# Performance work log

Measured on AMD Instinct MI355X. Metric: run time of the kernel, lower is better.

Reference implementation:

```python
import jax, jax.numpy as jnp
import numpy as np


def setup_inputs() -> dict:
    key = jax.random.key(0)
    ks = jax.random.split(key, 9)
    N, C, SY, SX = 256, 128, 11, 25
    DM, DC, D = 64, 64, 128
    return {
        "f_t_global": jax.random.normal(ks[0], (N, D), dtype=jnp.float32),
        "x_t_local": jax.random.normal(ks[1], (N, C, SY, SX), dtype=jnp.float32),
        "x_t_prev_local": jax.random.normal(ks[2], (N, C, SY, SX), dtype=jnp.float32),
        "m_t": jax.random.normal(ks[3], (N, DM), dtype=jnp.float32),
        "m_t_prev": jax.random.normal(ks[4], (N, DM), dtype=jnp.float32),
        "c_t": jax.random.normal(ks[5], (N, DC), dtype=jnp.float32),
        "c_t_prev": jax.random.normal(ks[6], (N, DC), dtype=jnp.float32),
        "W_join": jax.random.normal(ks[7], (C + DM + DC, D), dtype=jnp.float32) * 0.05,
        "b_join": jax.random.normal(ks[8], (D,), dtype=jnp.float32) * 0.05,
    }


def reference(f_t_global, x_t_local, x_t_prev_local, m_t, m_t_prev, c_t, c_t_prev, W_join, b_join):
    N, C, SY, SX = x_t_local.shape
    P = SY * SX
    DM = m_t.shape[1]
    # join_obs(local, m, c) = concat([local, m, c]) @ W_join + b_join, split for efficiency
    Wl = W_join[:C]                 # [C, D]
    Wm = W_join[C:C + DM]           # [DM, D]
    Wc = W_join[C + DM:]            # [DC, D]
    # [N, C, SY, SX] -> [P, N, C]: all spatial positions batched at once
    loc_t = x_t_local.reshape(N, C, P).transpose(2, 0, 1)
    loc_p = x_t_prev_local.reshape(N, C, P).transpose(2, 0, 1)
    bias_t = m_t @ Wm + c_t @ Wc + b_join             # [N, D], shared across positions
    bias_p = m_t_prev @ Wm + c_t_prev @ Wc + b_join   # [N, D]
    positive = jnp.einsum('pnc,cd->pnd', loc_p, Wl) + bias_p[None]  # [P, N, D]
    pred_loc = jnp.einsum('pnc,cd->pnd', loc_t, Wl) + bias_t[None]  # [P, N, D]

    # loss1: global prediction vs per-position prev-local positives
    logits1 = jnp.einsum('nd,pmd->pnm', f_t_global, positive)   # [P, N, N]
    # loss2: per-position current-local vs per-position prev-local
    logits2 = jnp.einsum('pnd,pmd->pnm', pred_loc, positive)    # [P, N, N]

    def mean_infonce(logits):
        # cross_entropy(logits, arange(N)) averaged over batch, then over positions
        lse = jax.nn.logsumexp(logits, axis=-1)            # [P, N]
        diag = jnp.diagonal(logits, axis1=1, axis2=2)      # [P, N]
        return jnp.mean(lse - diag)

    loss1 = mean_infonce(logits1)
    loss2 = mean_infonce(logits2)
    return loss1 + loss2
```

## Files before the change

kernel.cpp:

```cpp
#include <hip/hip_runtime.h>

#define Nn 256
#define Cc 128
#define Pp 275
#define Dd 128

typedef unsigned int u32;
typedef unsigned short u16;
typedef float f32x4 __attribute__((ext_vector_type(4)));
typedef short bf16x8 __attribute__((ext_vector_type(8)));

__device__ __forceinline__ float bf2f(u16 h) {
    return __uint_as_float(((u32)h) << 16);
}
__device__ __forceinline__ u16 f2bf(float f) {
    u32 u = __float_as_uint(f);
    return (u16)((u + 0x7fffu + ((u >> 16) & 1u)) >> 16);
}

__global__ __launch_bounds__(256) void bias_kernel(
    const float* __restrict__ m_t, const float* __restrict__ m_p,
    const float* __restrict__ c_t, const float* __restrict__ c_p,
    const float* __restrict__ W, const float* __restrict__ b,
    const float* __restrict__ f,
    float* __restrict__ bias_t, float* __restrict__ bias_p,
    u16* __restrict__ f_bf, u16* __restrict__ WlT)
{
    int idx = blockIdx.x * 256 + threadIdx.x;
    int n = idx >> 7, d = idx & 127;
    float at = 0.f, ap = 0.f;
#pragma unroll 8
    for (int k = 0; k < 64; ++k) {
        float wm = W[(128 + k) * 128 + d];
        float wc = W[(192 + k) * 128 + d];
        at = fmaf(m_t[n * 64 + k], wm, at);
        at = fmaf(c_t[n * 64 + k], wc, at);
        ap = fmaf(m_p[n * 64 + k], wm, ap);
        ap = fmaf(c_p[n * 64 + k], wc, ap);
    }
    float bb = b[d];
    bias_t[idx] = at + bb;
    bias_p[idx] = ap + bb;
    f_bf[idx] = f2bf(f[idx]);
    if (idx < 16384) {
        int dd = idx >> 7, cc = idx & 127;
        WlT[idx] = f2bf(W[cc * 128 + dd]);
    }
}

__global__ __launch_bounds__(512) void join_kernel512(
    const float* __restrict__ x_t, const float* __restrict__ x_p,
    const u16* __restrict__ WlT,
    const float* __restrict__ bias_t, const float* __restrict__ bias_p,
    u16* __restrict__ pred, u16* __restrict__ pos)
{
    __shared__ u16 lds[128 * 128];
    const int tid = threadIdx.x;
    const int n = blockIdx.x;
    const int w = tid >> 6;
    const int l = tid & 63;

    {
        const uint4* src = reinterpret_cast<const uint4*>(WlT);
#pragma unroll
        for (int it = 0; it < 4; ++it) {
            int j = tid + 512 * it;
            int row = j >> 4;
            int colb = (j & 15) << 4;
            uint4 v = src[j];
            *reinterpret_cast<uint4*>((char*)lds + row * 256 + (colb ^ ((row & 7) << 4))) = v;
        }
    }

    float bvT[8], bvP[8];
#pragma unroll
    for (int dt = 0; dt < 8; ++dt) {
        int d = dt * 16 + (l & 15);
        bvT[dt] = bias_t[n * 128 + d];
        bvP[dt] = bias_p[n * 128 + d];
    }

    __syncthreads();

    const float* xbase_t = x_t + (size_t)n * (Cc * Pp);
    const float* xbase_p = x_p + (size_t)n * (Cc * Pp);
    const int cg = (l >> 4) << 3;

    for (int t = w; t < 18; t += 8) {
        const int p0 = t * 16;
        int prow = p0 + (l & 15);
        if (prow > Pp - 1) prow = Pp - 1;
        const float* xs_t = xbase_t + prow;
        const float* xs_p = xbase_p + prow;

        bf16x8 At[4], Ap[4];
#pragma unroll
        for (int kk = 0; kk < 4; ++kk) {
            const size_t cb = (size_t)(kk * 32 + cg) * Pp;
            float vt[8], vp[8];
#pragma unroll
            for (int e = 0; e < 8; ++e) vt[e] = xs_t[cb + (size_t)e * Pp];
#pragma unroll
            for (int e = 0; e < 8; ++e) vp[e] = xs_p[cb + (size_t)e * Pp];
            bf16x8 a, c;
#pragma unroll
            for (int e = 0; e < 8; ++e) { a[e] = (short)f2bf(vt[e]); c[e] = (short)f2bf(vp[e]); }
            At[kk] = a;
            Ap[kk] = c;
        }

#pragma unroll
        for (int dt = 0; dt < 8; ++dt) {
            bf16x8 B[4];
            const int row = dt * 16 + (l & 15);
#pragma unroll
            for (int kk = 0; kk < 4; ++kk) {
                int cbyte = kk * 64 + ((l >> 4) << 4);
                B[kk] = *reinterpret_cast<const bf16x8*>(
                    (const char*)lds + row * 256 + (cbyte ^ ((row & 7) << 4)));
            }
            f32x4 aT = {0.f, 0.f, 0.f, 0.f}, aP = {0.f, 0.f, 0.f, 0.f};
#pragma unroll
            for (int kk = 0; kk < 4; ++kk) {
                aT = __builtin_amdgcn_mfma_f32_16x16x32_bf16(At[kk], B[kk], aT, 0, 0, 0);
                aP = __builtin_amdgcn_mfma_f32_16x16x32_bf16(Ap[kk], B[kk], aP, 0, 0, 0);
            }
            const int d = dt * 16 + (l & 15);
#pragma unroll
            for (int r = 0; r < 4; ++r) {
                int p = p0 + ((l >> 4) << 2) + r;
                if (p < Pp) {
                    size_t o = ((size_t)p * Nn + n) * Dd + d;
                    pred[o] = f2bf(aT[r] + bvT[dt]);
                    pos[o]  = f2bf(aP[r] + bvP[dt]);
                }
            }
        }
    }
}

__global__ __launch_bounds__(512) void logits_mfma_kernel(
    const u16* __restrict__ f_bf,
    const u16* __restrict__ pred, const u16* __restrict__ pos,
    float* __restrict__ partial)
{
    __shared__ u16 lds[Nn * Dd];
    const int tid = threadIdx.x;
    const int sel = blockIdx.x;
    const int p = blockIdx.y;
    const int w = tid >> 6;
    const int l = tid & 63;
    const int r0 = w * 32;

    {
        const uint4* src = reinterpret_cast<const uint4*>(pos + (size_t)p * (Nn * Dd));
#pragma unroll
        for (int it = 0; it < 8; ++it) {
            int j = tid + 512 * it;
            int row = j >> 4;
            int colb = (j & 15) << 4;
            uint4 v = src[j];
            *reinterpret_cast<uint4*>((char*)lds + row * 256 + (colb ^ ((row & 7) << 4))) = v;
        }
    }

    const u16* Abase = sel ? (pred + (size_t)p * (Nn * Dd)) : f_bf;
    bf16x8 A[2][4];
    {
        const int arow = l & 15;
        const int acol = (l >> 4) << 4;
#pragma unroll
        for (int rt = 0; rt < 2; ++rt)
#pragma unroll
            for (int kk = 0; kk < 4; ++kk) {
                const char* ap = (const char*)Abase
                               + (size_t)(r0 + rt * 16 + arow) * 256 + kk * 64 + acol;
                A[rt][kk] = *reinterpret_cast<const bf16x8*>(ap);
            }
    }

    __syncthreads();

    const float L2E = 1.4426950408889634f;
    float s_[2][4];
    float dg[2][4];
#pragma unroll
    for (int rt = 0; rt < 2; ++rt)
#pragma unroll
        for (int r = 0; r < 4; ++r) { s_[rt][r] = 0.f; dg[rt][r] = 0.f; }

    const int mcol = l & 15;
    const int bcol = (l >> 4) << 4;

    for (int ct = 0; ct < 16; ++ct) {
        bf16x8 B[4];
        const int mrow = ct * 16 + mcol;
#pragma unroll
        for (int kk = 0; kk < 4; ++kk) {
            int cb = kk * 64 + bcol;
            B[kk] = *reinterpret_cast<const bf16x8*>(
                (const char*)lds + mrow * 256 + (cb ^ ((mrow & 7) << 4)));
        }
#pragma unroll
        for (int rt = 0; rt < 2; ++rt) {
            f32x4 acc = {0.f, 0.f, 0.f, 0.f};
#pragma unroll
            for (int kk = 0; kk < 4; ++kk)
                acc = __builtin_amdgcn_mfma_f32_16x16x32_bf16(A[rt][kk], B[kk], acc, 0, 0, 0);
            const bool isdg_ct = (ct == ((r0 >> 4) + rt));
#pragma unroll
            for (int r = 0; r < 4; ++r) {
                float v = acc[r];
                s_[rt][r] += __builtin_amdgcn_exp2f(fmaf(v, L2E, -64.f));
                if (isdg_ct && ((l & 15) == (((l >> 4) << 2) + r))) dg[rt][r] = v;
            }
        }
    }

    float local = 0.f;
#pragma unroll
    for (int rt = 0; rt < 2; ++rt)
#pragma unroll
        for (int r = 0; r < 4; ++r) {
            float s = s_[rt][r];
            s += __shfl_xor(s, 1);
            s += __shfl_xor(s, 2);
            s += __shfl_xor(s, 4);
            s += __shfl_xor(s, 8);
            if ((l & 15) == (((l >> 4) << 2) + r))
                local += 0.6931471805599453f * (64.f + __log2f(s)) - dg[rt][r];
        }

    __syncthreads();
    float* red = reinterpret_cast<float*>(lds);
    red[tid] = local;
    __syncthreads();
    for (int k = 256; k > 0; k >>= 1) {
        if (tid < k) red[tid] += red[tid + k];
        __syncthreads();
    }
    if (tid == 0) partial[p * 2 + sel] = red[0];
}

__global__ __launch_bounds__(256) void reduce_kernel(
    const float* __restrict__ partial, float* __restrict__ out)
{
    __shared__ float red[256];
    float s = 0.f;
    for (int i = threadIdx.x; i < 2 * Pp; i += 256) s += partial[i];
    red[threadIdx.x] = s;
    __syncthreads();
    for (int k = 128; k > 0; k >>= 1) {
        if (threadIdx.x < k) red[threadIdx.x] += red[threadIdx.x + k];
        __syncthreads();
    }
    if (threadIdx.x == 0) out[0] = red[0] * (1.0f / (Pp * (float)Nn));
}

extern "C" void kernel_launch(void* const* d_in, const int* in_sizes, int n_in,
                              void* d_out, int out_size, void* d_ws, size_t ws_size,
                              hipStream_t stream)
{
    const float* f   = (const float*)d_in[0];
    const float* x_t = (const float*)d_in[1];
    const float* x_p = (const float*)d_in[2];
    const float* m_t = (const float*)d_in[3];
    const float* m_p = (const float*)d_in[4];
    const float* c_t = (const float*)d_in[5];
    const float* c_p = (const float*)d_in[6];
    const float* W   = (const float*)d_in[7];
    const float* b   = (const float*)d_in[8];

    char* ws = (char*)d_ws;
    const size_t SLAB = (size_t)Pp * Nn * Dd;

    float* bias_t = (float*)ws;
    float* bias_p = bias_t + Nn * Dd;
    u16* f_bf = (u16*)(ws + 262144);
    u16* WlT  = f_bf + Nn * Dd;
    u16* pred = (u16*)(ws + 360448);
    u16* pos  = pred + SLAB;
    float* partial = (float*)(pos + SLAB);

    bias_kernel<<<dim3(Nn * Dd / 256), 256, 0, stream>>>(m_t, m_p, c_t, c_p, W, b, f,
                                                         bias_t, bias_p, f_bf, WlT);
    join_kernel512<<<dim3(Nn), 512, 0, stream>>>(x_t, x_p, WlT, bias_t, bias_p,
                                                 pred, pos);
    logits_mfma_kernel<<<dim3(2, Pp), 512, 0, stream>>>(f_bf, pred, pos, partial);
    reduce_kernel<<<1, 256, 0, stream>>>(partial, (float*)d_out);
}
```

Baseline: 68.57 us.

## Software-pipeline join tile loads and merge both losses into one logits block

The join kernel is unrolled into explicit tile stages, so the global fp32 loads for the next spatial tile are issued before the MFMA work of the current tile, hiding load latency. The logits kernel now handles both losses for a position in a single block, with alternating waves taking loss1 and loss2 over 64 rows each. Each positive slab is therefore staged into LDS once instead of twice, and the grid shrinks by half. In exchange, register pressure rises from the prefetch buffers and the doubled A fragments, which may lower occupancy.

```diff
diff --git a/kernel.cpp b/kernel.cpp
--- a/kernel.cpp
+++ b/kernel.cpp
@@ -48,7 +48,70 @@
     }
 }
 
-__global__ __launch_bounds__(512) void join_kernel512(
+#define LOAD_TILE(vt, vp, t)                                          \
+    {                                                                 \
+        int prow_ = (t) * 16 + (l & 15);                              \
+        if (prow_ > Pp - 1) prow_ = Pp - 1;                           \
+        const float* xst_ = xb_t + prow_;                             \
+        const float* xsp_ = xb_p + prow_;                             \
+        _Pragma("unroll")                                             \
+        for (int kk = 0; kk < 4; ++kk) {                              \
+            const size_t cb_ = (size_t)(kk * 32 + cg) * Pp;           \
+            _Pragma("unroll")                                         \
+            for (int e = 0; e < 8; ++e) {                             \
+                vt[kk * 8 + e] = xst_[cb_ + (size_t)e * Pp];          \
+                vp[kk * 8 + e] = xsp_[cb_ + (size_t)e * Pp];          \
+            }                                                         \
+        }                                                             \
+    }
+
+#define CONV_TILE(At, Ap, vt, vp)                                     \
+    _Pragma("unroll")                                                 \
+    for (int kk = 0; kk < 4; ++kk) {                                  \
+        bf16x8 a_, c_;                                                \
+        _Pragma("unroll")                                             \
+        for (int e = 0; e < 8; ++e) {                                 \
+            a_[e] = (short)f2bf(vt[kk * 8 + e]);                      \
+            c_[e] = (short)f2bf(vp[kk * 8 + e]);                      \
+        }                                                             \
+        At[kk] = a_;                                                  \
+        Ap[kk] = c_;                                                  \
+    }
+
+#define COMPUTE_TILE(At, Ap, t)                                       \
+    {                                                                 \
+        const int p0_ = (t) * 16;                                     \
+        _Pragma("unroll")                                             \
+        for (int dt = 0; dt < 8; ++dt) {                              \
+            bf16x8 B_[4];                                             \
+            const int row_ = dt * 16 + (l & 15);                      \
+            _Pragma("unroll")                                         \
+            for (int kk = 0; kk < 4; ++kk) {                          \
+                int cbyte_ = kk * 64 + ((l >> 4) << 4);               \
+                B_[kk] = *reinterpret_cast<const bf16x8*>(            \
+                    (const char*)lds + row_ * 256 +                   \
+                    (cbyte_ ^ ((row_ & 7) << 4)));                    \
+            }                                                         \
+            f32x4 aT_ = {0.f,0.f,0.f,0.f}, aP_ = {0.f,0.f,0.f,0.f};   \
+            _Pragma("unroll")                                         \
+            for (int kk = 0; kk < 4; ++kk) {                          \
+                aT_ = __builtin_amdgcn_mfma_f32_16x16x32_bf16(At[kk], B_[kk], aT_, 0, 0, 0); \
+                aP_ = __builtin_amdgcn_mfma_f32_16x16x32_bf16(Ap[kk], B_[kk], aP_, 0, 0, 0); \
+            }                                                         \
+            const int d_ = dt * 16 + (l & 15);                        \
+            _Pragma("unroll")                                         \
+            for (int r = 0; r < 4; ++r) {                             \
+                int p_ = p0_ + ((l >> 4) << 2) + r;                   \
+                if (p_ < Pp) {                                        \
+                    size_t o_ = ((size_t)p_ * Nn + n) * Dd + d_;      \
+                    pred[o_] = f2bf(aT_[r] + bvT[dt]);                \
+                    pos[o_]  = f2bf(aP_[r] + bvP[dt]);                \
+                }                                                     \
+            }                                                         \
+        }                                                             \
+    }
+
+__global__ __launch_bounds__(512) void join_pipe_kernel(
     const float* __restrict__ x_t, const float* __restrict__ x_p,
     const u16* __restrict__ WlT,
     const float* __restrict__ bias_t, const float* __restrict__ bias_p,
@@ -72,6 +135,15 @@
         }
     }
 
+    const float* xb_t = x_t + (size_t)n * (Cc * Pp);
+    const float* xb_p = x_p + (size_t)n * (Cc * Pp);
+    const int cg = (l >> 4) << 3;
+
+    float vt0[32], vp0[32], vt1[32], vp1[32], vt2[32], vp2[32];
+    bf16x8 At0[4], Ap0[4], At1[4], Ap1[4], At2[4], Ap2[4];
+
+    LOAD_TILE(vt0, vp0, w);
+
     float bvT[8], bvP[8];
 #pragma unroll
     for (int dt = 0; dt < 8; ++dt) {
@@ -82,60 +154,15 @@
 
     __syncthreads();
 
-    const float* xbase_t = x_t + (size_t)n * (Cc * Pp);
-    const float* xbase_p = x_p + (size_t)n * (Cc * Pp);
-    const int cg = (l >> 4) << 3;
-
-    for (int t = w; t < 18; t += 8) {
-        const int p0 = t * 16;
-        int prow = p0 + (l & 15);
-        if (prow > Pp - 1) prow = Pp - 1;
-        const float* xs_t = xbase_t + prow;
-        const float* xs_p = xbase_p + prow;
-
-        bf16x8 At[4], Ap[4];
-#pragma unroll
-        for (int kk = 0; kk < 4; ++kk) {
-            const size_t cb = (size_t)(kk * 32 + cg) * Pp;
-            float vt[8], vp[8];
-#pragma unroll
-            for (int e = 0; e < 8; ++e) vt[e] = xs_t[cb + (size_t)e * Pp];
-#pragma unroll
-            for (int e = 0; e < 8; ++e) vp[e] = xs_p[cb + (size_t)e * Pp];
-            bf16x8 a, c;
-#pragma unroll
-            for (int e = 0; e < 8; ++e) { a[e] = (short)f2bf(vt[e]); c[e] = (short)f2bf(vp[e]); }
-            At[kk] = a;
-            Ap[kk] = c;
-        }
-
-#pragma unroll
-        for (int dt = 0; dt < 8; ++dt) {
-            bf16x8 B[4];
-            const int row = dt * 16 + (l & 15);
-#pragma unroll
-            for (int kk = 0; kk < 4; ++kk) {
-                int cbyte = kk * 64 + ((l >> 4) << 4);
-                B[kk] = *reinterpret_cast<const bf16x8*>(
-                    (const char*)lds + row * 256 + (cbyte ^ ((row & 7) << 4)));
-            }
-            f32x4 aT = {0.f, 0.f, 0.f, 0.f}, aP = {0.f, 0.f, 0.f, 0.f};
-#pragma unroll
-            for (int kk = 0; kk < 4; ++kk) {
-                aT = __builtin_amdgcn_mfma_f32_16x16x32_bf16(At[kk], B[kk], aT, 0, 0, 0);
-                aP = __builtin_amdgcn_mfma_f32_16x16x32_bf16(Ap[kk], B[kk], aP, 0, 0, 0);
-            }
-            const int d = dt * 16 + (l & 15);
-#pragma unroll
-            for (int r = 0; r < 4; ++r) {
-                int p = p0 + ((l >> 4) << 2) + r;
-                if (p < Pp) {
-                    size_t o = ((size_t)p * Nn + n) * Dd + d;
-                    pred[o] = f2bf(aT[r] + bvT[dt]);
-                    pos[o]  = f2bf(aP[r] + bvP[dt]);
-                }
-            }
-        }
+    CONV_TILE(At0, Ap0, vt0, vp0);
+    LOAD_TILE(vt1, vp1, w + 8);
+    COMPUTE_TILE(At0, Ap0, w);
+    CONV_TILE(At1, Ap1, vt1, vp1);
+    if (w < 2) LOAD_TILE(vt2, vp2, w + 16);
+    COMPUTE_TILE(At1, Ap1, w + 8);
+    if (w < 2) {
+        CONV_TILE(At2, Ap2, vt2, vp2);
+        COMPUTE_TILE(At2, Ap2, w + 16);
     }
 }
 
@@ -146,11 +173,11 @@
 {
     __shared__ u16 lds[Nn * Dd];
     const int tid = threadIdx.x;
-    const int sel = blockIdx.x;
-    const int p = blockIdx.y;
+    const int p = blockIdx.x;
     const int w = tid >> 6;
     const int l = tid & 63;
-    const int r0 = w * 32;
+    const int sel = w & 1;
+    const int r0 = (w >> 1) << 6;
 
     {
         const uint4* src = reinterpret_cast<const uint4*>(pos + (size_t)p * (Nn * Dd));
@@ -165,12 +192,12 @@
     }
 
     const u16* Abase = sel ? (pred + (size_t)p * (Nn * Dd)) : f_bf;
-    bf16x8 A[2][4];
+    bf16x8 A[4][4];
     {
         const int arow = l & 15;
         const int acol = (l >> 4) << 4;
 #pragma unroll
-        for (int rt = 0; rt < 2; ++rt)
+        for (int rt = 0; rt < 4; ++rt)
 #pragma unroll
             for (int kk = 0; kk < 4; ++kk) {
                 const char* ap = (const char*)Abase
@@ -182,10 +209,10 @@
     __syncthreads();
 
     const float L2E = 1.4426950408889634f;
-    float s_[2][4];
-    float dg[2][4];
-#pragma unroll
-    for (int rt = 0; rt < 2; ++rt)
+    float s_[4][4];
+    float dg[4][4];
+#pragma unroll
+    for (int rt = 0; rt < 4; ++rt)
 #pragma unroll
         for (int r = 0; r < 4; ++r) { s_[rt][r] = 0.f; dg[rt][r] = 0.f; }
 
@@ -202,7 +229,7 @@
                 (const char*)lds + mrow * 256 + (cb ^ ((mrow & 7) << 4)));
         }
 #pragma unroll
-        for (int rt = 0; rt < 2; ++rt) {
+        for (int rt = 0; rt < 4; ++rt) {
             f32x4 acc = {0.f, 0.f, 0.f, 0.f};
 #pragma unroll
             for (int kk = 0; kk < 4; ++kk)
@@ -219,7 +246,7 @@
 
     float local = 0.f;
 #pragma unroll
-    for (int rt = 0; rt < 2; ++rt)
+    for (int rt = 0; rt < 4; ++rt)
 #pragma unroll
         for (int r = 0; r < 4; ++r) {
             float s = s_[rt][r];
@@ -239,7 +266,7 @@
         if (tid < k) red[tid] += red[tid + k];
         __syncthreads();
     }
-    if (tid == 0) partial[p * 2 + sel] = red[0];
+    if (tid == 0) partial[p] = red[0];
 }
 
 __global__ __launch_bounds__(256) void reduce_kernel(
@@ -247,7 +274,7 @@
 {
     __shared__ float red[256];
     float s = 0.f;
-    for (int i = threadIdx.x; i < 2 * Pp; i += 256) s += partial[i];
+    for (int i = threadIdx.x; i < Pp; i += 256) s += partial[i];
     red[threadIdx.x] = s;
     __syncthreads();
     for (int k = 128; k > 0; k >>= 1) {
@@ -284,8 +311,8 @@
 
     bias_kernel<<<dim3(Nn * Dd / 256), 256, 0, stream>>>(m_t, m_p, c_t, c_p, W, b, f,
                                                          bias_t, bias_p, f_bf, WlT);
-    join_kernel512<<<dim3(Nn), 512, 0, stream>>>(x_t, x_p, WlT, bias_t, bias_p,
-                                                 pred, pos);
-    logits_mfma_kernel<<<dim3(2, Pp), 512, 0, stream>>>(f_bf, pred, pos, partial);
+    join_pipe_kernel<<<dim3(Nn), 512, 0, stream>>>(x_t, x_p, WlT, bias_t, bias_p,
+                                                   pred, pos);
+    logits_mfma_kernel<<<dim3(Pp), 512, 0, stream>>>(f_bf, pred, pos, partial);
     reduce_kernel<<<1, 256, 0, stream>>>(partial, (float*)d_out);
 }
```

New measurement: 74.20 us. 8.2% more time.

## Stage join-kernel input tiles through LDS with async double-buffered global_load_lds

Applied to the files above, without the earlier changes.

The join kernel now stages each 16-position tile of x through LDS using global_load_lds, double-buffered so the next tile loads while the current one is computed. Previously each lane issued strided scalar global loads straight into registers. The grid is also split into two halves per sample for more blocks, and each wave handles one of t/p and two of the eight D tiles instead of all of them. The last tile overlaps positions 259-274 so no bounds check is needed, which means some outputs are written twice with the same values. It adds a barrier per tile and extra LDS use.

```diff
diff --git a/kernel.cpp b/kernel.cpp
--- a/kernel.cpp
+++ b/kernel.cpp
@@ -16,6 +16,12 @@
 __device__ __forceinline__ u16 f2bf(float f) {
     u32 u = __float_as_uint(f);
     return (u16)((u + 0x7fffu + ((u >> 16) & 1u)) >> 16);
+}
+
+__device__ __forceinline__ void gload16(const float* g, float* l) {
+    __builtin_amdgcn_global_load_lds(
+        (const __attribute__((address_space(1))) void*)g,
+        (__attribute__((address_space(3))) void*)l, 16, 0, 0);
 }
 
 __global__ __launch_bounds__(256) void bias_kernel(
@@ -48,17 +54,20 @@
     }
 }
 
-__global__ __launch_bounds__(512) void join_kernel512(
+__global__ __launch_bounds__(512) void join_gl_kernel(
     const float* __restrict__ x_t, const float* __restrict__ x_p,
     const u16* __restrict__ WlT,
     const float* __restrict__ bias_t, const float* __restrict__ bias_p,
     u16* __restrict__ pred, u16* __restrict__ pos)
 {
-    __shared__ u16 lds[128 * 128];
+    __shared__ u16 wlds[128 * 128];
+    __shared__ float xbuf[2][4096];
     const int tid = threadIdx.x;
-    const int n = blockIdx.x;
+    const int half = blockIdx.x;
+    const int n = blockIdx.y;
     const int w = tid >> 6;
     const int l = tid & 63;
+    const int g = l >> 4;
 
     {
         const uint4* src = reinterpret_cast<const uint4*>(WlT);
@@ -68,74 +77,84 @@
             int row = j >> 4;
             int colb = (j & 15) << 4;
             uint4 v = src[j];
-            *reinterpret_cast<uint4*>((char*)lds + row * 256 + (colb ^ ((row & 7) << 4))) = v;
-        }
-    }
-
-    float bvT[8], bvP[8];
-#pragma unroll
-    for (int dt = 0; dt < 8; ++dt) {
-        int d = dt * 16 + (l & 15);
-        bvT[dt] = bias_t[n * 128 + d];
-        bvP[dt] = bias_p[n * 128 + d];
-    }
-
-    __syncthreads();
-
-    const float* xbase_t = x_t + (size_t)n * (Cc * Pp);
-    const float* xbase_p = x_p + (size_t)n * (Cc * Pp);
-    const int cg = (l >> 4) << 3;
-
-    for (int t = w; t < 18; t += 8) {
-        const int p0 = t * 16;
-        int prow = p0 + (l & 15);
-        if (prow > Pp - 1) prow = Pp - 1;
-        const float* xs_t = xbase_t + prow;
-        const float* xs_p = xbase_p + prow;
-
-        bf16x8 At[4], Ap[4];
+            *reinterpret_cast<uint4*>((char*)wlds + row * 256 + (colb ^ ((row & 7) << 4))) = v;
+        }
+    }
+
+    const float* xbt = x_t + (size_t)n * (Cc * Pp);
+    const float* xbp = x_p + (size_t)n * (Cc * Pp);
+
+    const int dt0 = w >> 1;
+    const float* bias = (w & 1) ? bias_p : bias_t;
+    u16* outp = (w & 1) ? pos : pred;
+    float bv0 = bias[n * 128 + dt0 * 16 + (l & 15)];
+    float bv1 = bias[n * 128 + (dt0 + 4) * 16 + (l & 15)];
+
+    const int sc = (w << 4) + (l >> 2);
+    const int sp = (l & 3) << 2;
+
+    {
+        const int t0 = half * 9;
+        const int p0 = (t0 < 17) ? t0 * 16 : 259;
+        const size_t go = (size_t)sc * Pp + p0 + sp;
+        gload16(xbt + go, &xbuf[0][w * 256]);
+        gload16(xbp + go, &xbuf[0][2048 + w * 256]);
+    }
+    __syncthreads();
+
+    int ib = 0;
+    for (int tt = 0; tt < 9; ++tt) {
+        const int tcur = half * 9 + tt;
+        const int p0 = (tcur < 17) ? tcur * 16 : 259;
+        if (tt < 8) {
+            const int tn = tcur + 1;
+            const int pn = (tn < 17) ? tn * 16 : 259;
+            const size_t go = (size_t)sc * Pp + pn + sp;
+            gload16(xbt + go, &xbuf[ib ^ 1][w * 256]);
+            gload16(xbp + go, &xbuf[ib ^ 1][2048 + w * 256]);
+        }
+
+        const float* xb = &xbuf[ib][(w & 1) * 2048];
+        bf16x8 A[4];
 #pragma unroll
         for (int kk = 0; kk < 4; ++kk) {
-            const size_t cb = (size_t)(kk * 32 + cg) * Pp;
-            float vt[8], vp[8];
-#pragma unroll
-            for (int e = 0; e < 8; ++e) vt[e] = xs_t[cb + (size_t)e * Pp];
-#pragma unroll
-            for (int e = 0; e < 8; ++e) vp[e] = xs_p[cb + (size_t)e * Pp];
-            bf16x8 a, c;
-#pragma unroll
-            for (int e = 0; e < 8; ++e) { a[e] = (short)f2bf(vt[e]); c[e] = (short)f2bf(vp[e]); }
-            At[kk] = a;
-            Ap[kk] = c;
-        }
-
-#pragma unroll
-        for (int dt = 0; dt < 8; ++dt) {
+            bf16x8 a;
+#pragma unroll
+            for (int j = 0; j < 8; ++j) {
+                const int e = (j + g) & 7;
+                const int c = kk * 32 + g * 8 + e;
+                float v = xb[((c >> 4) << 8) + ((c & 15) << 4) + (l & 15)];
+                a[e] = (short)f2bf(v);
+            }
+            A[kk] = a;
+        }
+
+#pragma unroll
+        for (int i = 0; i < 2; ++i) {
+            const int dt = dt0 + i * 4;
             bf16x8 B[4];
             const int row = dt * 16 + (l & 15);
 #pragma unroll
             for (int kk = 0; kk < 4; ++kk) {
-                int cbyte = kk * 64 + ((l >> 4) << 4);
+                int cbyte = kk * 64 + (g << 4);
                 B[kk] = *reinterpret_cast<const bf16x8*>(
-                    (const char*)lds + row * 256 + (cbyte ^ ((row & 7) << 4)));
-            }
-            f32x4 aT = {0.f, 0.f, 0.f, 0.f}, aP = {0.f, 0.f, 0.f, 0.f};
-#pragma unroll
-            for (int kk = 0; kk < 4; ++kk) {
-                aT = __builtin_amdgcn_mfma_f32_16x16x32_bf16(At[kk], B[kk], aT, 0, 0, 0);
-                aP = __builtin_amdgcn_mfma_f32_16x16x32_bf16(Ap[kk], B[kk], aP, 0, 0, 0);
-            }
+                    (const char*)wlds + row * 256 + (cbyte ^ ((row & 7) << 4)));
+            }
+            f32x4 acc = {0.f, 0.f, 0.f, 0.f};
+#pragma unroll
+            for (int kk = 0; kk < 4; ++kk)
+                acc = __builtin_amdgcn_mfma_f32_16x16x32_bf16(A[kk], B[kk], acc, 0, 0, 0);
             const int d = dt * 16 + (l & 15);
+            const float bv = i ? bv1 : bv0;
 #pragma unroll
             for (int r = 0; r < 4; ++r) {
-                int p = p0 + ((l >> 4) << 2) + r;
-                if (p < Pp) {
-                    size_t o = ((size_t)p * Nn + n) * Dd + d;
-                    pred[o] = f2bf(aT[r] + bvT[dt]);
-                    pos[o]  = f2bf(aP[r] + bvP[dt]);
-                }
-            }
-        }
+                const int p = p0 + g * 4 + r;
+                outp[((size_t)p * Nn + n) * Dd + d] = f2bf(acc[r] + bv);
+            }
+        }
+
+        __syncthreads();
+        ib ^= 1;
     }
 }
 
@@ -284,8 +303,8 @@
 
     bias_kernel<<<dim3(Nn * Dd / 256), 256, 0, stream>>>(m_t, m_p, c_t, c_p, W, b, f,
                                                          bias_t, bias_p, f_bf, WlT);
-    join_kernel512<<<dim3(Nn), 512, 0, stream>>>(x_t, x_p, WlT, bias_t, bias_p,
-                                                 pred, pos);
+    join_gl_kernel<<<dim3(2, Nn), 512, 0, stream>>>(x_t, x_p, WlT, bias_t, bias_p,
+                                                    pred, pos);
     logits_mfma_kernel<<<dim3(2, Pp), 512, 0, stream>>>(f_bf, pred, pos, partial);
     reduce_kernel<<<1, 256, 0, stream>>>(partial, (float*)d_out);
 }
```

After: 109.3 us. +59.4%, slower.
